# Performance work log

Hardware: AMD Instinct MI355X
Metric: run time of the kernel (lower is better)

## Reference

```python
import jax, jax.numpy as jnp
import numpy as np

BERT_DIM = 768
N_ROWS = 5
N_COLS = 12
LN_EPS = 1e-5


def setup_inputs() -> dict:
    key = jax.random.key(0)
    ks = jax.random.split(key, 12)
    B, S = 256, 512
    token_hidden = jax.random.normal(ks[0], (B, S, BERT_DIM), dtype=jnp.float32)
    attention_mask = jax.random.randint(ks[1], (B, S), 0, 2, dtype=jnp.int32)
    s = lambda fan_in: 1.0 / np.sqrt(fan_in)
    return {
        "token_hidden": token_hidden,
        "attention_mask": attention_mask,
        # token_attention: Linear(768,128) -> Tanh -> Linear(128,1)
        "att_w1": jax.random.normal(ks[2], (128, BERT_DIM), dtype=jnp.float32) * s(BERT_DIM),
        "att_b1": jnp.zeros((128,), dtype=jnp.float32),
        "att_w2": jax.random.normal(ks[3], (1, 128), dtype=jnp.float32) * s(128),
        "att_b2": jnp.zeros((1,), dtype=jnp.float32),
        # feature_projector: Linear(768,256) -> GELU -> Dropout(eval) -> Linear(256,5)
        "proj_w1": jax.random.normal(ks[4], (256, BERT_DIM), dtype=jnp.float32) * s(BERT_DIM),
        "proj_b1": jnp.zeros((256,), dtype=jnp.float32),
        "proj_w2": jax.random.normal(ks[5], (N_ROWS, 256), dtype=jnp.float32) * s(256),
        "proj_b2": jnp.zeros((N_ROWS,), dtype=jnp.float32),
        # LayerNorm([5, 12])
        "ln_gamma": jnp.ones((N_ROWS, N_COLS), dtype=jnp.float32),
        "ln_beta": jnp.zeros((N_ROWS, N_COLS), dtype=jnp.float32),
    }


def reference(token_hidden, attention_mask, att_w1, att_b1, att_w2, att_b2,
              proj_w1, proj_b1, proj_w2, proj_b2, ln_gamma, ln_beta):
    # token attention scores: [B, S]
    h = jnp.tanh(jnp.einsum("bsd,hd->bsh", token_hidden, att_w1) + att_b1)
    scores = (jnp.einsum("bsh,oh->bso", h, att_w2) + att_b2)[..., 0]
    scores = jnp.where(attention_mask == 0, jnp.finfo(scores.dtype).min, scores)
    weights = jax.nn.softmax(scores, axis=-1)
    # top-k token selection (indices sorted ascending to preserve order)
    k = min(N_COLS, token_hidden.shape[1])
    _, top_idx = jax.lax.top_k(weights, k)  # [B, k]
    top_idx = jnp.sort(top_idx, axis=-1)
    selected = jnp.take_along_axis(token_hidden, top_idx[:, :, None], axis=1)  # [B, k, D]
    # feature projector (dropout is eval no-op)
    f = jax.nn.gelu(jnp.einsum("bkd,hd->bkh", selected, proj_w1) + proj_b1, approximate=False)
    f = jnp.einsum("bkh,rh->bkr", f, proj_w2) + proj_b2  # [B, k, n_rows]
    features = jnp.transpose(f, (0, 2, 1))  # [B, n_rows, k]
    if features.shape[-1] < N_COLS:
        features = jnp.pad(features, ((0, 0), (0, 0), (0, N_COLS - features.shape[-1])))
    # LayerNorm over trailing [n_rows, n_cols]
    mean = jnp.mean(features, axis=(-2, -1), keepdims=True)
    var = jnp.var(features, axis=(-2, -1), keepdims=True)
    return ln_gamma * (features - mean) * jax.lax.rsqrt(var + LN_EPS) + ln_beta
```

## Files before the change

kernel.cpp:

```cpp
#include <hip/hip_runtime.h>
#include <math.h>

#define B_BATCH 256
#define S_LEN   512
#define D_DIM   768
#define H_ATT   128
#define TOPK    12
#define NCAND   16
#define H_PROJ  256
#define N_ROWS  5
#define N_COLS  12

typedef __bf16 bf16x8 __attribute__((ext_vector_type(8)));
typedef float  f32x4  __attribute__((ext_vector_type(4)));

__device__ inline void split8(float4 a, float4 b, bf16x8& hi, bf16x8& lo) {
    float v[8] = {a.x, a.y, a.z, a.w, b.x, b.y, b.z, b.w};
#pragma unroll
    for (int i = 0; i < 8; ++i) {
        __bf16 h = (__bf16)v[i];
        hi[i] = h;
        lo[i] = (__bf16)(v[i] - (float)h);
    }
}

__global__ __launch_bounds__(512, 2) void fused_kernel(
    const float* __restrict__ th,
    const int*   __restrict__ mask,
    const float* __restrict__ aw1,
    const float* __restrict__ ab1,
    const float* __restrict__ aw2,
    const float* __restrict__ pw1,
    const float* __restrict__ pb1,
    const float* __restrict__ pw2,
    const float* __restrict__ pb2,
    const float* __restrict__ gamma,
    const float* __restrict__ beta,
    float* __restrict__ out)
{
    const int b   = blockIdx.x;
    const int tid = threadIdx.x;
    const int wv  = tid >> 6;
    const int ln  = tid & 63;

    __shared__ float score_s[S_LEN];
    __shared__ float4 xc[NCAND][192];
    __shared__ unsigned long long wtop[128];
    __shared__ int   cand[NCAND];
    __shared__ float redW[8][4];
    __shared__ float exact_sc[NCAND];
    __shared__ int   sel_slot[TOPK];
    __shared__ float gbuf[TOPK][H_PROJ + 4];
    __shared__ float feat[N_ROWS * N_COLS];
    __shared__ float stats[2];

    const float NEG_MIN = -3.402823466e38f;

    const int col = ln & 15;
    const int kq  = ln >> 4;

    for (int g = 0; g < 2; ++g) {
        const size_t row0 = (size_t)b * S_LEN + g * 256 + wv * 32 + col;
        const float* pa0 = th + row0 * D_DIM + kq * 8;
        const float* pa1 = pa0 + 16 * D_DIM;

        f32x4 acc[2][8];
        const f32x4 z = {0.f, 0.f, 0.f, 0.f};
#pragma unroll
        for (int i = 0; i < 2; ++i)
#pragma unroll
            for (int j = 0; j < 8; ++j) acc[i][j] = z;

        float4 c00 = *(const float4*)(pa0);
        float4 c01 = *(const float4*)(pa0 + 4);
        float4 c10 = *(const float4*)(pa1);
        float4 c11 = *(const float4*)(pa1 + 4);
        float4 bc[8][2];
#pragma unroll
        for (int nt = 0; nt < 8; ++nt) {
            const float* pb = aw1 + (size_t)(nt * 16 + col) * D_DIM + kq * 8;
            bc[nt][0] = *(const float4*)(pb);
            bc[nt][1] = *(const float4*)(pb + 4);
        }

        for (int kt = 0; kt < 24; ++kt) {
            float4 n00, n01, n10, n11;
            float4 bn[8][2];
            if (kt < 23) {
                n00 = *(const float4*)(pa0 + (kt + 1) * 32);
                n01 = *(const float4*)(pa0 + (kt + 1) * 32 + 4);
                n10 = *(const float4*)(pa1 + (kt + 1) * 32);
                n11 = *(const float4*)(pa1 + (kt + 1) * 32 + 4);
#pragma unroll
                for (int nt = 0; nt < 8; ++nt) {
                    const float* pb = aw1 + (size_t)(nt * 16 + col) * D_DIM +
                                      (kt + 1) * 32 + kq * 8;
                    bn[nt][0] = *(const float4*)(pb);
                    bn[nt][1] = *(const float4*)(pb + 4);
                }
            }

            bf16x8 ah0, al0, ah1, al1;
            split8(c00, c01, ah0, al0);
            split8(c10, c11, ah1, al1);

#pragma unroll
            for (int nt = 0; nt < 8; ++nt) {
                bf16x8 bh, bl;
                split8(bc[nt][0], bc[nt][1], bh, bl);
                acc[0][nt] = __builtin_amdgcn_mfma_f32_16x16x32_bf16(ah0, bh, acc[0][nt], 0, 0, 0);
                acc[0][nt] = __builtin_amdgcn_mfma_f32_16x16x32_bf16(al0, bh, acc[0][nt], 0, 0, 0);
                acc[0][nt] = __builtin_amdgcn_mfma_f32_16x16x32_bf16(ah0, bl, acc[0][nt], 0, 0, 0);
                acc[1][nt] = __builtin_amdgcn_mfma_f32_16x16x32_bf16(ah1, bh, acc[1][nt], 0, 0, 0);
                acc[1][nt] = __builtin_amdgcn_mfma_f32_16x16x32_bf16(al1, bh, acc[1][nt], 0, 0, 0);
                acc[1][nt] = __builtin_amdgcn_mfma_f32_16x16x32_bf16(ah1, bl, acc[1][nt], 0, 0, 0);
            }

            if (kt < 23) {
                c00 = n00; c01 = n01; c10 = n10; c11 = n11;
#pragma unroll
                for (int nt = 0; nt < 8; ++nt) {
                    bc[nt][0] = bn[nt][0];
                    bc[nt][1] = bn[nt][1];
                }
            }
        }

        float b1v[8], w2v[8];
#pragma unroll
        for (int nt = 0; nt < 8; ++nt) {
            b1v[nt] = ab1[nt * 16 + col];
            w2v[nt] = aw2[nt * 16 + col];
        }
        const int rowbase = g * 256 + wv * 32;
#pragma unroll
        for (int mf = 0; mf < 2; ++mf)
#pragma unroll
            for (int r = 0; r < 4; ++r) {
                float s = 0.f;
#pragma unroll
                for (int nt = 0; nt < 8; ++nt)
                    s += tanhf(acc[mf][nt][r] + b1v[nt]) * w2v[nt];
                s += __shfl_xor(s, 1, 64);
                s += __shfl_xor(s, 2, 64);
                s += __shfl_xor(s, 4, 64);
                s += __shfl_xor(s, 8, 64);
                if (col == 0)
                    score_s[rowbase + mf * 16 + kq * 4 + r] = s;
            }
    }
    __syncthreads();

    {
        int i0 = wv * 64 + ln;
        float v0 = score_s[i0];
        if (mask[(size_t)b * S_LEN + i0] == 0) v0 = NEG_MIN;
        unsigned k0 = __float_as_uint(v0);
        k0 = ((int)k0 >= 0) ? (k0 | 0x80000000u) : ~k0;
        unsigned long long p0 =
            ((unsigned long long)k0 << 32) | (0xFFFFFFFFu - (unsigned)i0);
        for (int it = 0; it < NCAND; ++it) {
            unsigned long long m = p0;
#pragma unroll
            for (int s = 1; s <= 32; s <<= 1) {
                unsigned long long o = __shfl_xor(m, s, 64);
                if (o > m) m = o;
            }
            if (ln == 0) wtop[wv * 16 + it] = m;
            if (p0 == m) p0 = 0ull;
        }
    }
    __syncthreads();
    if (wv == 0) {
        unsigned long long p0 = wtop[ln];
        unsigned long long p1 = wtop[64 + ln];
        for (int it = 0; it < NCAND; ++it) {
            unsigned long long m = p0 > p1 ? p0 : p1;
#pragma unroll
            for (int s = 1; s <= 32; s <<= 1) {
                unsigned long long o = __shfl_xor(m, s, 64);
                if (o > m) m = o;
            }
            if (ln == 0) cand[it] = (int)(0xFFFFFFFFu - (unsigned)(m & 0xFFFFFFFFu));
            if (p0 == m) p0 = 0ull;
            else if (p1 == m) p1 = 0ull;
        }
    }
    __syncthreads();

#pragma unroll
    for (int i = 0; i < 6; ++i) {
        int f = tid + 512 * i;
        int c = f / 192, k4 = f % 192;
        xc[c][k4] = *(const float4*)(th + ((size_t)b * S_LEN + cand[c]) * D_DIM + k4 * 4);
    }
    __syncthreads();

    {
        const int n = tid & 127;
        const int h = tid >> 7;
        float accs[4] = {0.f, 0.f, 0.f, 0.f};
        const float* wrow = aw1 + (size_t)n * D_DIM;
        for (int k4 = 0; k4 < 192; ++k4) {
            float4 w = *(const float4*)(wrow + k4 * 4);
#pragma unroll
            for (int j = 0; j < 4; ++j) {
                float4 x = xc[4 * h + j][k4];
                accs[j] += w.x * x.x + w.y * x.y + w.z * x.z + w.w * x.w;
            }
        }
        float b1n = ab1[n], w2n = aw2[n];
#pragma unroll
        for (int j = 0; j < 4; ++j) {
            float val = tanhf(accs[j] + b1n) * w2n;
            val += __shfl_xor(val, 1, 64);
            val += __shfl_xor(val, 2, 64);
            val += __shfl_xor(val, 4, 64);
            val += __shfl_xor(val, 8, 64);
            val += __shfl_xor(val, 16, 64);
            val += __shfl_xor(val, 32, 64);
            if (ln == 0) redW[wv][j] = val;
        }
    }
    __syncthreads();
    if (tid < NCAND) {
        int c = tid, h = c >> 2, j = c & 3;
        float ex = redW[2 * h][j] + redW[2 * h + 1][j];
        if (mask[(size_t)b * S_LEN + cand[c]] == 0) ex = -INFINITY;
        exact_sc[c] = ex;
    }
    __syncthreads();

    if (tid == 0) {
        unsigned picked = 0;
        int slots[TOPK];
        for (int it = 0; it < TOPK; ++it) {
            float best = -INFINITY; int bslot = -1; int bidx = 1 << 30;
            for (int c = 0; c < NCAND; ++c) {
                if (picked & (1u << c)) continue;
                float e = exact_sc[c]; int idx = cand[c];
                if (e > best || (e == best && idx < bidx)) { best = e; bslot = c; bidx = idx; }
            }
            picked |= 1u << bslot;
            slots[it] = bslot;
        }
        for (int i = 1; i < TOPK; ++i) {
            int s = slots[i], key = cand[s], j = i - 1;
            while (j >= 0 && cand[slots[j]] > key) { slots[j + 1] = slots[j]; --j; }
            slots[j + 1] = s;
        }
        for (int t = 0; t < TOPK; ++t) sel_slot[t] = slots[t];
    }
    __syncthreads();

    {
        const int j  = tid & 255;
        const int hh = tid >> 8;
        int slots[6];
#pragma unroll
        for (int t = 0; t < 6; ++t) slots[t] = sel_slot[hh * 6 + t];
        float accp[6];
        float bj = pb1[j];
#pragma unroll
        for (int t = 0; t < 6; ++t) accp[t] = bj;
        const float* wrow = pw1 + (size_t)j * D_DIM;
        for (int k4 = 0; k4 < 192; ++k4) {
            float4 w = *(const float4*)(wrow + k4 * 4);
#pragma unroll
            for (int t = 0; t < 6; ++t) {
                float4 x = xc[slots[t]][k4];
                accp[t] += w.x * x.x + w.y * x.y + w.z * x.z + w.w * x.w;
            }
        }
#pragma unroll
        for (int t = 0; t < 6; ++t) {
            float hv = accp[t];
            gbuf[hh * 6 + t][j] = 0.5f * hv * (1.0f + erff(hv * 0.70710678118654752f));
        }
    }
    __syncthreads();

    if (tid < TOPK * N_ROWS) {
        int t = tid / N_ROWS, r = tid % N_ROWS;
        float s = pb2[r];
        const float4* gp = (const float4*)&gbuf[t][0];
        const float4* wp = (const float4*)(pw2 + r * H_PROJ);
        for (int q = 0; q < H_PROJ / 4; ++q) {
            float4 g = gp[q], w = wp[q];
            s += g.x * w.x + g.y * w.y + g.z * w.z + g.w * w.w;
        }
        feat[r * N_COLS + t] = s;
    }
    __syncthreads();

    if (tid == 0) {
        float sum = 0.f;
        for (int i = 0; i < N_ROWS * N_COLS; ++i) sum += feat[i];
        float mean = sum / 60.f;
        float sq = 0.f;
        for (int i = 0; i < N_ROWS * N_COLS; ++i) { float d = feat[i] - mean; sq += d * d; }
        stats[0] = mean;
        stats[1] = sq / 60.f;
    }
    __syncthreads();
    if (tid < N_ROWS * N_COLS) {
        float x = feat[tid];
        out[(size_t)b * 60 + tid] =
            gamma[tid] * (x - stats[0]) * rsqrtf(stats[1] + 1e-5f) + beta[tid];
    }
}

extern "C" void kernel_launch(void* const* d_in, const int* in_sizes, int n_in,
                              void* d_out, int out_size, void* d_ws, size_t ws_size,
                              hipStream_t stream) {
    const float* th   = (const float*)d_in[0];
    const int*   mask = (const int*)  d_in[1];
    const float* aw1  = (const float*)d_in[2];
    const float* ab1  = (const float*)d_in[3];
    const float* aw2  = (const float*)d_in[4];
    const float* pw1  = (const float*)d_in[6];
    const float* pb1  = (const float*)d_in[7];
    const float* pw2  = (const float*)d_in[8];
    const float* pb2  = (const float*)d_in[9];
    const float* gam  = (const float*)d_in[10];
    const float* bet  = (const float*)d_in[11];
    float* out = (float*)d_out;

    (void)d_ws; (void)ws_size;

    hipLaunchKernelGGL(fused_kernel, dim3(B_BATCH), dim3(512), 0, stream,
                       th, mask, aw1, ab1, aw2, pw1, pb1, pw2, pb2,
                       gam, bet, out);
}
```

Measured before the change: 788.4 us.

## Stage split bf16 attention weights in shared memory and double block size

Each block now runs 1024 threads, so the 512 tokens are covered in a single pass instead of two. The attention weight tile is converted to hi/lo bf16 once per k-step and written into a double-buffered shared-memory buffer. Before, every wave reloaded the weight rows from global memory and re-split them itself. The shared buffer is aliased with the candidate-row buffer, and the later phases are repartitioned across the larger block. This removes redundant weight loads and conversions, at the cost of a barrier every k-step and heavier per-thread register limits.

```diff
diff --git a/kernel.cpp b/kernel.cpp
--- a/kernel.cpp
+++ b/kernel.cpp
@@ -12,6 +12,7 @@
 #define N_COLS  12
 
 typedef __bf16 bf16x8 __attribute__((ext_vector_type(8)));
+typedef __bf16 bf16x4 __attribute__((ext_vector_type(4)));
 typedef float  f32x4  __attribute__((ext_vector_type(4)));
 
 __device__ inline void split8(float4 a, float4 b, bf16x8& hi, bf16x8& lo) {
@@ -24,7 +25,7 @@
     }
 }
 
-__global__ __launch_bounds__(512, 2) void fused_kernel(
+__global__ __launch_bounds__(1024, 4) void fused_kernel(
     const float* __restrict__ th,
     const int*   __restrict__ mask,
     const float* __restrict__ aw1,
@@ -43,11 +44,14 @@
     const int wv  = tid >> 6;
     const int ln  = tid & 63;
 
+    __shared__ __align__(16) char ubuf[49152];
+    __bf16 (*Bs)[2][4096] = reinterpret_cast<__bf16 (*)[2][4096]>(ubuf);
+    float4 (*xc)[192]     = reinterpret_cast<float4 (*)[192]>(ubuf);
+
     __shared__ float score_s[S_LEN];
-    __shared__ float4 xc[NCAND][192];
     __shared__ unsigned long long wtop[128];
     __shared__ int   cand[NCAND];
-    __shared__ float redW[8][4];
+    __shared__ float redW[16][2];
     __shared__ float exact_sc[NCAND];
     __shared__ int   sel_slot[TOPK];
     __shared__ float gbuf[TOPK][H_PROJ + 4];
@@ -56,83 +60,89 @@
 
     const float NEG_MIN = -3.402823466e38f;
 
+    auto build = [&](int kt, int buf) {
+        const int nt = tid >> 7;
+        const int r  = tid & 127;
+        const int l2 = r >> 1;
+        const int h4 = (r & 1) * 4;
+        const float* src = aw1 + (size_t)(nt * 16 + (l2 & 15)) * D_DIM +
+                           kt * 32 + (l2 >> 4) * 8 + h4;
+        float4 v = *(const float4*)src;
+        bf16x4 hv, lv;
+#pragma unroll
+        for (int i = 0; i < 4; ++i) {
+            float f = (&v.x)[i];
+            __bf16 hb = (__bf16)f;
+            hv[i] = hb;
+            lv[i] = (__bf16)(f - (float)hb);
+        }
+        const int base = nt * 512 + l2 * 8 + h4;
+        *(bf16x4*)(&Bs[buf][0][base]) = hv;
+        *(bf16x4*)(&Bs[buf][1][base]) = lv;
+    };
+
     const int col = ln & 15;
     const int kq  = ln >> 4;
 
-    for (int g = 0; g < 2; ++g) {
-        const size_t row0 = (size_t)b * S_LEN + g * 256 + wv * 32 + col;
-        const float* pa0 = th + row0 * D_DIM + kq * 8;
-        const float* pa1 = pa0 + 16 * D_DIM;
-
-        f32x4 acc[2][8];
-        const f32x4 z = {0.f, 0.f, 0.f, 0.f};
-#pragma unroll
-        for (int i = 0; i < 2; ++i)
-#pragma unroll
-            for (int j = 0; j < 8; ++j) acc[i][j] = z;
-
-        float4 c00 = *(const float4*)(pa0);
-        float4 c01 = *(const float4*)(pa0 + 4);
-        float4 c10 = *(const float4*)(pa1);
-        float4 c11 = *(const float4*)(pa1 + 4);
-        float4 bc[8][2];
+    const size_t row0 = (size_t)b * S_LEN + wv * 32 + col;
+    const float* pa0 = th + row0 * D_DIM + kq * 8;
+    const float* pa1 = pa0 + 16 * D_DIM;
+
+    f32x4 acc[2][8];
+    const f32x4 z = {0.f, 0.f, 0.f, 0.f};
+#pragma unroll
+    for (int i = 0; i < 2; ++i)
+#pragma unroll
+        for (int j = 0; j < 8; ++j) acc[i][j] = z;
+
+    float4 c00 = *(const float4*)(pa0);
+    float4 c01 = *(const float4*)(pa0 + 4);
+    float4 c10 = *(const float4*)(pa1);
+    float4 c11 = *(const float4*)(pa1 + 4);
+    build(0, 0);
+    __syncthreads();
+
+    for (int kt = 0; kt < 24; ++kt) {
+        const int buf = kt & 1;
+        float4 n00, n01, n10, n11;
+        if (kt < 23) {
+            n00 = *(const float4*)(pa0 + (kt + 1) * 32);
+            n01 = *(const float4*)(pa0 + (kt + 1) * 32 + 4);
+            n10 = *(const float4*)(pa1 + (kt + 1) * 32);
+            n11 = *(const float4*)(pa1 + (kt + 1) * 32 + 4);
+            build(kt + 1, buf ^ 1);
+        }
+
+        bf16x8 ah0, al0, ah1, al1;
+        split8(c00, c01, ah0, al0);
+        split8(c10, c11, ah1, al1);
+
 #pragma unroll
         for (int nt = 0; nt < 8; ++nt) {
-            const float* pb = aw1 + (size_t)(nt * 16 + col) * D_DIM + kq * 8;
-            bc[nt][0] = *(const float4*)(pb);
-            bc[nt][1] = *(const float4*)(pb + 4);
-        }
-
-        for (int kt = 0; kt < 24; ++kt) {
-            float4 n00, n01, n10, n11;
-            float4 bn[8][2];
-            if (kt < 23) {
-                n00 = *(const float4*)(pa0 + (kt + 1) * 32);
-                n01 = *(const float4*)(pa0 + (kt + 1) * 32 + 4);
-                n10 = *(const float4*)(pa1 + (kt + 1) * 32);
-                n11 = *(const float4*)(pa1 + (kt + 1) * 32 + 4);
-#pragma unroll
-                for (int nt = 0; nt < 8; ++nt) {
-                    const float* pb = aw1 + (size_t)(nt * 16 + col) * D_DIM +
-                                      (kt + 1) * 32 + kq * 8;
-                    bn[nt][0] = *(const float4*)(pb);
-                    bn[nt][1] = *(const float4*)(pb + 4);
-                }
-            }
-
-            bf16x8 ah0, al0, ah1, al1;
-            split8(c00, c01, ah0, al0);
-            split8(c10, c11, ah1, al1);
-
-#pragma unroll
-            for (int nt = 0; nt < 8; ++nt) {
-                bf16x8 bh, bl;
-                split8(bc[nt][0], bc[nt][1], bh, bl);
-                acc[0][nt] = __builtin_amdgcn_mfma_f32_16x16x32_bf16(ah0, bh, acc[0][nt], 0, 0, 0);
-                acc[0][nt] = __builtin_amdgcn_mfma_f32_16x16x32_bf16(al0, bh, acc[0][nt], 0, 0, 0);
-                acc[0][nt] = __builtin_amdgcn_mfma_f32_16x16x32_bf16(ah0, bl, acc[0][nt], 0, 0, 0);
-                acc[1][nt] = __builtin_amdgcn_mfma_f32_16x16x32_bf16(ah1, bh, acc[1][nt], 0, 0, 0);
-                acc[1][nt] = __builtin_amdgcn_mfma_f32_16x16x32_bf16(al1, bh, acc[1][nt], 0, 0, 0);
-                acc[1][nt] = __builtin_amdgcn_mfma_f32_16x16x32_bf16(ah1, bl, acc[1][nt], 0, 0, 0);
-            }
-
-            if (kt < 23) {
-                c00 = n00; c01 = n01; c10 = n10; c11 = n11;
-#pragma unroll
-                for (int nt = 0; nt < 8; ++nt) {
-                    bc[nt][0] = bn[nt][0];
-                    bc[nt][1] = bn[nt][1];
-                }
-            }
-        }
-
+            bf16x8 bh = *(bf16x8*)(&Bs[buf][0][nt * 512 + ln * 8]);
+            bf16x8 bl = *(bf16x8*)(&Bs[buf][1][nt * 512 + ln * 8]);
+            acc[0][nt] = __builtin_amdgcn_mfma_f32_16x16x32_bf16(ah0, bh, acc[0][nt], 0, 0, 0);
+            acc[0][nt] = __builtin_amdgcn_mfma_f32_16x16x32_bf16(al0, bh, acc[0][nt], 0, 0, 0);
+            acc[0][nt] = __builtin_amdgcn_mfma_f32_16x16x32_bf16(ah0, bl, acc[0][nt], 0, 0, 0);
+            acc[1][nt] = __builtin_amdgcn_mfma_f32_16x16x32_bf16(ah1, bh, acc[1][nt], 0, 0, 0);
+            acc[1][nt] = __builtin_amdgcn_mfma_f32_16x16x32_bf16(al1, bh, acc[1][nt], 0, 0, 0);
+            acc[1][nt] = __builtin_amdgcn_mfma_f32_16x16x32_bf16(ah1, bl, acc[1][nt], 0, 0, 0);
+        }
+
+        if (kt < 23) {
+            c00 = n00; c01 = n01; c10 = n10; c11 = n11;
+            __syncthreads();
+        }
+    }
+
+    {
         float b1v[8], w2v[8];
 #pragma unroll
         for (int nt = 0; nt < 8; ++nt) {
             b1v[nt] = ab1[nt * 16 + col];
             w2v[nt] = aw2[nt * 16 + col];
         }
-        const int rowbase = g * 256 + wv * 32;
+        const int rowbase = wv * 32;
 #pragma unroll
         for (int mf = 0; mf < 2; ++mf)
 #pragma unroll
@@ -151,7 +161,7 @@
     }
     __syncthreads();
 
-    {
+    if (wv < 8) {
         int i0 = wv * 64 + ln;
         float v0 = score_s[i0];
         if (mask[(size_t)b * S_LEN + i0] == 0) v0 = NEG_MIN;
@@ -189,29 +199,29 @@
     __syncthreads();
 
 #pragma unroll
-    for (int i = 0; i < 6; ++i) {
-        int f = tid + 512 * i;
+    for (int i = 0; i < 3; ++i) {
+        int f = tid + 1024 * i;
         int c = f / 192, k4 = f % 192;
         xc[c][k4] = *(const float4*)(th + ((size_t)b * S_LEN + cand[c]) * D_DIM + k4 * 4);
     }
     __syncthreads();
 
     {
-        const int n = tid & 127;
-        const int h = tid >> 7;
-        float accs[4] = {0.f, 0.f, 0.f, 0.f};
+        const int n  = tid & 127;
+        const int h8 = tid >> 7;
+        float accs[2] = {0.f, 0.f};
         const float* wrow = aw1 + (size_t)n * D_DIM;
         for (int k4 = 0; k4 < 192; ++k4) {
             float4 w = *(const float4*)(wrow + k4 * 4);
 #pragma unroll
-            for (int j = 0; j < 4; ++j) {
-                float4 x = xc[4 * h + j][k4];
+            for (int j = 0; j < 2; ++j) {
+                float4 x = xc[2 * h8 + j][k4];
                 accs[j] += w.x * x.x + w.y * x.y + w.z * x.z + w.w * x.w;
             }
         }
         float b1n = ab1[n], w2n = aw2[n];
 #pragma unroll
-        for (int j = 0; j < 4; ++j) {
+        for (int j = 0; j < 2; ++j) {
             float val = tanhf(accs[j] + b1n) * w2n;
             val += __shfl_xor(val, 1, 64);
             val += __shfl_xor(val, 2, 64);
@@ -224,8 +234,9 @@
     }
     __syncthreads();
     if (tid < NCAND) {
-        int c = tid, h = c >> 2, j = c & 3;
-        float ex = redW[2 * h][j] + redW[2 * h + 1][j];
+        int c = tid;
+        int wbase = c & ~1;
+        float ex = redW[wbase][c & 1] + redW[wbase + 1][c & 1];
         if (mask[(size_t)b * S_LEN + cand[c]] == 0) ex = -INFINITY;
         exact_sc[c] = ex;
     }
@@ -256,26 +267,26 @@
     {
         const int j  = tid & 255;
         const int hh = tid >> 8;
-        int slots[6];
-#pragma unroll
-        for (int t = 0; t < 6; ++t) slots[t] = sel_slot[hh * 6 + t];
-        float accp[6];
+        int slots[3];
+#pragma unroll
+        for (int t = 0; t < 3; ++t) slots[t] = sel_slot[hh * 3 + t];
+        float accp[3];
         float bj = pb1[j];
 #pragma unroll
-        for (int t = 0; t < 6; ++t) accp[t] = bj;
+        for (int t = 0; t < 3; ++t) accp[t] = bj;
         const float* wrow = pw1 + (size_t)j * D_DIM;
         for (int k4 = 0; k4 < 192; ++k4) {
             float4 w = *(const float4*)(wrow + k4 * 4);
 #pragma unroll
-            for (int t = 0; t < 6; ++t) {
+            for (int t = 0; t < 3; ++t) {
                 float4 x = xc[slots[t]][k4];
                 accp[t] += w.x * x.x + w.y * x.y + w.z * x.z + w.w * x.w;
             }
         }
 #pragma unroll
-        for (int t = 0; t < 6; ++t) {
+        for (int t = 0; t < 3; ++t) {
             float hv = accp[t];
-            gbuf[hh * 6 + t][j] = 0.5f * hv * (1.0f + erff(hv * 0.70710678118654752f));
+            gbuf[hh * 3 + t][j] = 0.5f * hv * (1.0f + erff(hv * 0.70710678118654752f));
         }
     }
     __syncthreads();
@@ -328,7 +339,7 @@
 
     (void)d_ws; (void)ws_size;
 
-    hipLaunchKernelGGL(fused_kernel, dim3(B_BATCH), dim3(512), 0, stream,
+    hipLaunchKernelGGL(fused_kernel, dim3(B_BATCH), dim3(1024), 0, stream,
                        th, mask, aw1, ab1, aw2, pw1, pb1, pw2, pb2,
                        gam, bet, out);
 }
```

After: 762.7 us. 1.03x faster.
